# Kernel tuning notes

Hardware: AMD Instinct MI355X
Metric: run time of the kernel (lower is better)

Reference implementation:

```python
import jax, jax.numpy as jnp
import numpy as np

B, C, H_IMG, W_IMG = 16, 384, 56, 56
NUM_HEADS = 6
HEAD_DIM = C // NUM_HEADS
BN_EPS = 1e-5


def _bn(x, gamma, beta, mean, var):
    # x: [b, ch, n] or [b, ch, h, w]; per-channel affine normalization (eval-mode BatchNorm)
    shape = (1, -1) + (1,) * (x.ndim - 2)
    scale = (gamma / jnp.sqrt(var + BN_EPS)).reshape(shape)
    shift = (beta - mean * gamma / jnp.sqrt(var + BN_EPS)).reshape(shape)
    return x * scale + shift


def setup_inputs() -> dict:
    key = jax.random.key(0)
    ks = jax.random.split(key, 12)
    c2 = 2 * C
    return {
        "x": jax.random.normal(ks[0], (B, C, H_IMG, W_IMG), jnp.float32),
        "qk_w": jax.random.normal(ks[1], (c2, C // 2), jnp.float32) * 0.05,
        "qk_gamma": jax.random.uniform(ks[2], (c2,), jnp.float32, 0.5, 1.5),
        "qk_beta": jax.random.normal(ks[3], (c2,), jnp.float32) * 0.1,
        "qk_mean": jax.random.normal(ks[4], (c2,), jnp.float32) * 0.1,
        "qk_var": jax.random.uniform(ks[5], (c2,), jnp.float32, 0.5, 1.5),
        "pe_w": jax.random.normal(ks[6], (C, 1, 3, 3), jnp.float32) * 0.1,
        "pe_gamma": jax.random.uniform(ks[7], (C,), jnp.float32, 0.5, 1.5),
        "pe_beta": jax.random.normal(ks[8], (C,), jnp.float32) * 0.1,
        "pe_mean": jax.random.normal(ks[9], (C,), jnp.float32) * 0.1,
        "pe_var": jax.random.uniform(ks[10], (C,), jnp.float32, 0.5, 1.5),
    }


def reference(x, qk_w, qk_gamma, qk_beta, qk_mean, qk_var,
              pe_w, pe_gamma, pe_beta, pe_mean, pe_var):
    b, c, h, w = x.shape
    n = h * w
    s = n ** (-0.5)
    nh, hd = NUM_HEADS, HEAD_DIM

    # grouped (groups=2) 1x1 conv: out channels [0:c] from input [0:c/2], [c:2c] from [c/2:c]
    xg = x.reshape(b, 2, c // 2, n)                       # [b, 2, c/2, n]
    wg = qk_w.reshape(2, c, c // 2)                       # [group, out_per_group, in_per_group]
    qk = jnp.einsum('bgin,goi->bgon', xg, wg).reshape(b, 2 * c, n)
    qk = _bn(qk, qk_gamma, qk_beta, qk_mean, qk_var)
    qk = jax.nn.elu(qk) + 1.0

    qk = qk.reshape(b, 2, nh, hd, n)
    q, k = qk[:, 0], qk[:, 1]                             # [b, H, d, n]
    v = x.reshape(b, nh, hd, n)                           # [b, H, d, n]

    # kv = (k*s) @ (v^T * s): [b, H, d, d]
    kv = jnp.einsum('bhdn,bhen->bhde', k * s, v * s)
    # numerator: q^T @ kv -> [b, H, n, d]
    num = jnp.einsum('bhdn,bhde->bhne', q, kv)
    # denominator: q^T @ mean_n(k) -> [b, H, n]
    den = jnp.einsum('bhdn,bhd->bhn', q, k.mean(axis=-1)) + 1e-6
    attn = (num / den[..., None]).transpose(0, 1, 3, 2).reshape(b, c, h, w)

    # depthwise 3x3 conv positional encoding on v (= x) + BN
    pe = jax.lax.conv_general_dilated(
        x, pe_w, window_strides=(1, 1), padding=((1, 1), (1, 1)),
        feature_group_count=c, dimension_numbers=('NCHW', 'OIHW', 'NCHW'))
    pe = _bn(pe, pe_gamma, pe_beta, pe_mean, pe_var)

    return attn + pe
```

## Files before the change

kernel.cpp:

```cpp
#include <hip/hip_runtime.h>
#include <math.h>

#define N_SP 3136
#define BN_EPS 1e-5f

typedef __attribute__((ext_vector_type(8))) short short8;
typedef __attribute__((ext_vector_type(4))) float f32x4;

#define QK_SZ   (16*2*384*N_SP)
#define KVP_OFF (QK_SZ)
#define KVP_SZ  (16*6*7*64*64)
#define KMP_OFF (KVP_OFF + KVP_SZ)
#define KMP_SZ  (16*6*7*64)
#define KV_OFF  (KMP_OFF + KMP_SZ)
#define KV_SZ   (16*6*64*64)
#define KM_OFF  (KV_OFF + KV_SZ)
#define KM_SZ   (16*6*64)
#define WH_OFF  (KM_OFF + KM_SZ)
#define WSPLIT_N (2*384*192)

__device__ __forceinline__ void bsplit(float f, ushort& h, ushort& l) {
    uint u = __float_as_uint(f);
    uint hr = (u + 0x7FFFu + ((u >> 16) & 1u)) >> 16;
    h = (ushort)hr;
    float fh = __uint_as_float(hr << 16);
    float fl = f - fh;
    uint v = __float_as_uint(fl);
    l = (ushort)((v + 0x7FFFu + ((v >> 16) & 1u)) >> 16);
}

__global__ __launch_bounds__(256) void p0_wsplit(
    const float* __restrict__ qk_w, ushort* __restrict__ wh, ushort* __restrict__ wl)
{
    int idx = blockIdx.x * 256 + threadIdx.x;
    if (idx >= WSPLIT_N) return;
    ushort h, l;
    bsplit(qk_w[idx], h, l);
    wh[idx] = h;
    wl[idx] = l;
}

__global__ __launch_bounds__(256) void k1_qk_mfma(
    const float* __restrict__ x, const ushort* __restrict__ wh, const ushort* __restrict__ wl,
    const float* __restrict__ gamma, const float* __restrict__ beta,
    const float* __restrict__ mean, const float* __restrict__ var,
    float* __restrict__ qk_out)
{
    __shared__ __align__(16) ushort Ah[8192];
    __shared__ __align__(16) ushort Al[8192];
    __shared__ __align__(16) ushort Bh[4096];
    __shared__ __align__(16) ushort Bl[4096];

    const int bx = blockIdx.x;
    const int by = blockIdx.y;
    const int bz = blockIdx.z;
    const int b = bz >> 1, gg = bz & 1;
    const int t = threadIdx.x;
    const int lane = t & 63, wv = t >> 6;
    const int wr = wv >> 1, wc = wv & 1;
    const int lg = lane >> 4, l15 = lane & 15;

    f32x4 acc[4][2];
    #pragma unroll
    for (int m = 0; m < 4; ++m)
        #pragma unroll
        for (int nf = 0; nf < 2; ++nf)
            acc[m][nf] = (f32x4){0.f, 0.f, 0.f, 0.f};

    const float* xg = x + (size_t)(b * 384 + gg * 192) * N_SP + bx * 64;
    const ushort* whg = wh + (gg * 384 + by * 128) * 192;
    const ushort* wlg = wl + (gg * 384 + by * 128) * 192;

    for (int kt = 0; kt < 3; ++kt) {
        #pragma unroll
        for (int li = 0; li < 4; ++li) {
            int c = li * 256 + t;
            int row = c >> 3, kb = c & 7;
            int goff = row * 192 + kt * 64 + kb * 8;
            float4 vh = *(const float4*)(whg + goff);
            float4 vl = *(const float4*)(wlg + goff);
            int ch = (row * 8 + (kb ^ (row & 7))) * 8;
            *(float4*)&Ah[ch] = vh;
            *(float4*)&Al[ch] = vl;
        }
        #pragma unroll
        for (int li = 0; li < 2; ++li) {
            int idx = li * 256 + t;
            int kp = idx >> 4;
            int nq = idx & 15;
            int k0 = kp * 2;
            const float* px = xg + (size_t)(kt * 64 + k0) * N_SP + nq * 4;
            float4 v0 = *(const float4*)px;
            float4 v1 = *(const float4*)(px + N_SP);
            ushort h0[4], l0[4], h1[4], l1[4];
            float a0[4] = {v0.x, v0.y, v0.z, v0.w};
            float a1[4] = {v1.x, v1.y, v1.z, v1.w};
            #pragma unroll
            for (int i = 0; i < 4; ++i) { bsplit(a0[i], h0[i], l0[i]); bsplit(a1[i], h1[i], l1[i]); }
            int kb = k0 >> 3, ks = (k0 & 6) >> 1;
            #pragma unroll
            for (int i = 0; i < 4; ++i) {
                int n = nq * 4 + i;
                int chunk = n * 8 + (kb ^ ((n >> 1) & 7));
                ((uint*)Bh)[chunk * 4 + ks] = (uint)h0[i] | ((uint)h1[i] << 16);
                ((uint*)Bl)[chunk * 4 + ks] = (uint)l0[i] | ((uint)l1[i] << 16);
            }
        }
        __syncthreads();
        #pragma unroll
        for (int s = 0; s < 2; ++s) {
            short8 ah[4], al[4], bh[2], bl[2];
            int kb = s * 4 + lg;
            #pragma unroll
            for (int m = 0; m < 4; ++m) {
                int row = wr * 64 + m * 16 + l15;
                int ch = (row * 8 + (kb ^ (row & 7))) * 8;
                ah[m] = *(const short8*)&Ah[ch];
                al[m] = *(const short8*)&Al[ch];
            }
            #pragma unroll
            for (int nf = 0; nf < 2; ++nf) {
                int n = wc * 32 + nf * 16 + l15;
                int ch = (n * 8 + (kb ^ ((n >> 1) & 7))) * 8;
                bh[nf] = *(const short8*)&Bh[ch];
                bl[nf] = *(const short8*)&Bl[ch];
            }
            #pragma unroll
            for (int m = 0; m < 4; ++m)
                #pragma unroll
                for (int nf = 0; nf < 2; ++nf) {
                    acc[m][nf] = __builtin_amdgcn_mfma_f32_16x16x32_bf16(ah[m], bh[nf], acc[m][nf], 0, 0, 0);
                    acc[m][nf] = __builtin_amdgcn_mfma_f32_16x16x32_bf16(ah[m], bl[nf], acc[m][nf], 0, 0, 0);
                    acc[m][nf] = __builtin_amdgcn_mfma_f32_16x16x32_bf16(al[m], bh[nf], acc[m][nf], 0, 0, 0);
                }
        }
        __syncthreads();
    }

    float* scs = (float*)Bh;
    float* shs = scs + 128;
    if (t < 128) {
        int ch = gg * 384 + by * 128 + t;
        float sc = gamma[ch] / sqrtf(var[ch] + BN_EPS);
        scs[t] = sc;
        shs[t] = beta[ch] - mean[ch] * sc;
    }
    __syncthreads();

    size_t obase = ((size_t)(b * 2 + gg) * 384 + by * 128) * N_SP + bx * 64 + wc * 32;
    #pragma unroll
    for (int m = 0; m < 4; ++m)
        #pragma unroll
        for (int nf = 0; nf < 2; ++nf) {
            #pragma unroll
            for (int r = 0; r < 4; ++r) {
                int orow = wr * 64 + m * 16 + lg * 4 + r;
                float v = acc[m][nf][r] * scs[orow] + shs[orow];
                v = v > 0.f ? v + 1.f : __expf(v);
                qk_out[obase + (size_t)orow * N_SP + nf * 16 + l15] = v;
            }
        }
}

__global__ __launch_bounds__(256) void k2_kv(
    const float* __restrict__ x, const float* __restrict__ qk,
    float* __restrict__ kv_part, float* __restrict__ km_part)
{
    __shared__ float ks[64][68];
    __shared__ float vs[64][68];
    const int chunk = blockIdx.x;
    const int h = blockIdx.y, b = blockIdx.z;
    const int t = threadIdx.x, tx = t & 15, ty = t >> 4;
    const float* kp = qk + ((b*2+1)*384 + h*64)*N_SP;
    const float* vp = x  + (b*384 + h*64)*N_SP;
    float acc[4][4] = {};
    float kmacc[4] = {};
    for (int sub = 0; sub < 7; ++sub) {
        int n0 = chunk*448 + sub*64;
        #pragma unroll
        for (int l = 0; l < 4; ++l) {
            int idx = t + l*256;
            int d = idx >> 4, c = idx & 15;
            float4 v4 = *(const float4*)&kp[d*N_SP + n0 + c*4];
            ks[c*4+0][d] = v4.x; ks[c*4+1][d] = v4.y;
            ks[c*4+2][d] = v4.z; ks[c*4+3][d] = v4.w;
        }
        #pragma unroll
        for (int l = 0; l < 4; ++l) {
            int idx = t + l*256;
            int e = idx >> 4, c = idx & 15;
            float4 v4 = *(const float4*)&vp[e*N_SP + n0 + c*4];
            vs[c*4+0][e] = v4.x; vs[c*4+1][e] = v4.y;
            vs[c*4+2][e] = v4.z; vs[c*4+3][e] = v4.w;
        }
        __syncthreads();
        #pragma unroll 8
        for (int n = 0; n < 64; ++n) {
            float4 kd = *(const float4*)&ks[n][ty*4];
            float4 ve = *(const float4*)&vs[n][tx*4];
            float kk[4] = {kd.x,kd.y,kd.z,kd.w}, vv[4] = {ve.x,ve.y,ve.z,ve.w};
            #pragma unroll
            for (int i = 0; i < 4; ++i) {
                kmacc[i] += kk[i];
                #pragma unroll
                for (int j = 0; j < 4; ++j) acc[i][j] += kk[i]*vv[j];
            }
        }
        __syncthreads();
    }
    const int base = ((b*6+h)*7 + chunk)*4096;
    #pragma unroll
    for (int i = 0; i < 4; ++i) {
        float4 r = make_float4(acc[i][0], acc[i][1], acc[i][2], acc[i][3]);
        *(float4*)&kv_part[base + (ty*4+i)*64 + tx*4] = r;
    }
    if (tx == 0) {
        const int kb = ((b*6+h)*7 + chunk)*64;
        #pragma unroll
        for (int i = 0; i < 4; ++i) km_part[kb + ty*4+i] = kmacc[i];
    }
}

__global__ __launch_bounds__(256) void k2b_reduce(
    const float* __restrict__ kv_part, const float* __restrict__ km_part,
    float* __restrict__ kv, float* __restrict__ km)
{
    int idx = blockIdx.x*256 + threadIdx.x;
    const float inv_n = 1.0f / (float)N_SP;
    if (idx < 16*6*64*64) {
        int bh = idx >> 12, de = idx & 4095;
        float s = 0.f;
        #pragma unroll
        for (int c = 0; c < 7; ++c) s += kv_part[(bh*7+c)*4096 + de];
        kv[idx] = s * inv_n;
    }
    if (idx < 16*6*64) {
        int bh = idx >> 6, d = idx & 63;
        float s = 0.f;
        #pragma unroll
        for (int c = 0; c < 7; ++c) s += km_part[(bh*7+c)*64 + d];
        km[idx] = s * inv_n;
    }
}

__global__ __launch_bounds__(256) void k3_attn_pe(
    const float* __restrict__ x, const float* __restrict__ qk,
    const float* __restrict__ kv, const float* __restrict__ km,
    const float* __restrict__ pw,
    const float* __restrict__ pgamma, const float* __restrict__ pbeta,
    const float* __restrict__ pmean, const float* __restrict__ pvar,
    float* __restrict__ out)
{
    __shared__ float qs[64][68];
    __shared__ float kvs[64][68];
    __shared__ float kms[64];
    const int bx = blockIdx.x;
    const int h = blockIdx.y, b = blockIdx.z;
    const int t = threadIdx.x, tx = t & 15, ty = t >> 4;
    const int n0 = bx*64;
    const float* qp  = qk + ((b*2+0)*384 + h*64)*N_SP;
    const float* kvp = kv + (b*6+h)*4096;
    #pragma unroll
    for (int l = 0; l < 4; ++l) {
        int idx = t + l*256;
        int d = idx >> 4, c = idx & 15;
        *(float4*)&qs[d][c*4] = *(const float4*)&qp[d*N_SP + n0 + c*4];
    }
    #pragma unroll
    for (int l = 0; l < 4; ++l) {
        int idx = t + l*256;
        int d = idx >> 4, c = idx & 15;
        *(float4*)&kvs[d][c*4] = *(const float4*)&kvp[d*64 + c*4];
    }
    if (t < 64) kms[t] = km[(b*6+h)*64 + t];
    __syncthreads();

    float acc[4][4] = {};
    float den[4] = {};
    #pragma unroll 8
    for (int d = 0; d < 64; ++d) {
        float4 qn = *(const float4*)&qs[d][tx*4];
        float4 ke = *(const float4*)&kvs[d][ty*4];
        float qq[4] = {qn.x,qn.y,qn.z,qn.w}, kk[4] = {ke.x,ke.y,ke.z,ke.w};
        float kmd = kms[d];
        #pragma unroll
        for (int p = 0; p < 4; ++p) {
            den[p] += qq[p]*kmd;
            #pragma unroll
            for (int j = 0; j < 4; ++j) acc[p][j] += qq[p]*kk[j];
        }
    }

    const int p0 = n0 + tx*4;
    const int y = p0 / 56, xc = p0 % 56;
    #pragma unroll
    for (int j = 0; j < 4; ++j) {
        int c = h*64 + ty*4 + j;
        const float* xp = x + ((size_t)b*384 + c)*N_SP;
        float seg[3][6];
        #pragma unroll
        for (int dy = 0; dy < 3; ++dy) {
            int yy = y + dy - 1;
            bool yok = (yy >= 0) && (yy < 56);
            const float* xr = xp + yy*56;
            #pragma unroll
            for (int s = 0; s < 6; ++s) {
                int col = xc - 1 + s;
                seg[dy][s] = (yok && col >= 0 && col < 56) ? xr[col] : 0.f;
            }
        }
        float w9[9];
        #pragma unroll
        for (int q = 0; q < 9; ++q) w9[q] = pw[c*9 + q];
        float sc2 = pgamma[c] / sqrtf(pvar[c] + BN_EPS);
        float sh2 = pbeta[c] - pmean[c]*sc2;
        float4 r;
        float* pr = (float*)&r;
        #pragma unroll
        for (int p = 0; p < 4; ++p) {
            float conv = 0.f;
            #pragma unroll
            for (int dy = 0; dy < 3; ++dy)
                #pragma unroll
                for (int dx = 0; dx < 3; ++dx)
                    conv += w9[dy*3+dx] * seg[dy][p + dx];
            pr[p] = acc[p][j] / (den[p] + 1e-6f) + (conv*sc2 + sh2);
        }
        *(float4*)&out[((size_t)b*384 + c)*N_SP + p0] = r;
    }
}

extern "C" void kernel_launch(void* const* d_in, const int* in_sizes, int n_in,
                              void* d_out, int out_size, void* d_ws, size_t ws_size,
                              hipStream_t stream)
{
    const float* x        = (const float*)d_in[0];
    const float* qk_w     = (const float*)d_in[1];
    const float* qk_gamma = (const float*)d_in[2];
    const float* qk_beta  = (const float*)d_in[3];
    const float* qk_mean  = (const float*)d_in[4];
    const float* qk_var   = (const float*)d_in[5];
    const float* pe_w     = (const float*)d_in[6];
    const float* pe_gamma = (const float*)d_in[7];
    const float* pe_beta  = (const float*)d_in[8];
    const float* pe_mean  = (const float*)d_in[9];
    const float* pe_var   = (const float*)d_in[10];
    float* out = (float*)d_out;

    float* ws      = (float*)d_ws;
    float* qk      = ws;
    float* kv_part = ws + KVP_OFF;
    float* km_part = ws + KMP_OFF;
    float* kv      = ws + KV_OFF;
    float* km      = ws + KM_OFF;
    ushort* whp    = (ushort*)(ws + WH_OFF);
    ushort* wlp    = whp + WSPLIT_N;

    hipLaunchKernelGGL(p0_wsplit, dim3((WSPLIT_N + 255)/256), dim3(256), 0, stream,
                       qk_w, whp, wlp);
    dim3 g1(49, 3, 32);
    hipLaunchKernelGGL(k1_qk_mfma, g1, dim3(256), 0, stream,
                       x, whp, wlp, qk_gamma, qk_beta, qk_mean, qk_var, qk);
    dim3 g2(7, 6, 16);
    hipLaunchKernelGGL(k2_kv, g2, dim3(256), 0, stream, x, qk, kv_part, km_part);
    hipLaunchKernelGGL(k2b_reduce, dim3(1536), dim3(256), 0, stream,
                       kv_part, km_part, kv, km);
    dim3 g3(49, 6, 16);
    hipLaunchKernelGGL(k3_attn_pe, g3, dim3(256), 0, stream,
                       x, qk, kv, km, pe_w, pe_gamma, pe_beta, pe_mean, pe_var, out);
}
```

Baseline: 241.9 us.

## Compute KV with split-bf16 MFMA, fold k-mean into ones column, vectorize PE loads

```diff
diff --git a/kernel.cpp b/kernel.cpp
--- a/kernel.cpp
+++ b/kernel.cpp
@@ -9,10 +9,8 @@
 
 #define QK_SZ   (16*2*384*N_SP)
 #define KVP_OFF (QK_SZ)
-#define KVP_SZ  (16*6*7*64*64)
-#define KMP_OFF (KVP_OFF + KVP_SZ)
-#define KMP_SZ  (16*6*7*64)
-#define KV_OFF  (KMP_OFF + KMP_SZ)
+#define KVP_SZ  (16*6*7*64*80)
+#define KV_OFF  (KVP_OFF + KVP_SZ)
 #define KV_SZ   (16*6*64*64)
 #define KM_OFF  (KV_OFF + KV_SZ)
 #define KM_SZ   (16*6*64)
@@ -162,83 +160,106 @@
         }
 }
 
-__global__ __launch_bounds__(256) void k2_kv(
+__global__ __launch_bounds__(256) void k2_kv_mfma(
     const float* __restrict__ x, const float* __restrict__ qk,
-    float* __restrict__ kv_part, float* __restrict__ km_part)
-{
-    __shared__ float ks[64][68];
-    __shared__ float vs[64][68];
+    float* __restrict__ kv_part)
+{
+    __shared__ __align__(16) ushort Kh[4096], Kl[4096];
+    __shared__ __align__(16) ushort Vh[5120], Vl[5120];
+
     const int chunk = blockIdx.x;
     const int h = blockIdx.y, b = blockIdx.z;
-    const int t = threadIdx.x, tx = t & 15, ty = t >> 4;
-    const float* kp = qk + ((b*2+1)*384 + h*64)*N_SP;
-    const float* vp = x  + (b*384 + h*64)*N_SP;
-    float acc[4][4] = {};
-    float kmacc[4] = {};
+    const int t = threadIdx.x;
+    const int lane = t & 63, wv = t >> 6;
+    const int lg = lane >> 4, l15 = lane & 15;
+
+    const float* kp = qk + (size_t)((b*2+1)*384 + h*64) * N_SP;
+    const float* vp = x  + (size_t)(b*384 + h*64) * N_SP;
+
+    #pragma unroll
+    for (int li = 0; li < 4; ++li) {
+        int idx = li * 256 + t;
+        int row = 64 + (idx >> 6), col = idx & 63;
+        int off = (row * 8 + ((col >> 3) ^ (row & 7))) * 8 + (col & 7);
+        Vh[off] = (row == 64) ? (ushort)0x3F80 : (ushort)0;
+        Vl[off] = 0;
+    }
+
+    f32x4 acc[5];
+    #pragma unroll
+    for (int nf = 0; nf < 5; ++nf) acc[nf] = (f32x4){0.f, 0.f, 0.f, 0.f};
+
     for (int sub = 0; sub < 7; ++sub) {
-        int n0 = chunk*448 + sub*64;
-        #pragma unroll
-        for (int l = 0; l < 4; ++l) {
-            int idx = t + l*256;
-            int d = idx >> 4, c = idx & 15;
-            float4 v4 = *(const float4*)&kp[d*N_SP + n0 + c*4];
-            ks[c*4+0][d] = v4.x; ks[c*4+1][d] = v4.y;
-            ks[c*4+2][d] = v4.z; ks[c*4+3][d] = v4.w;
-        }
-        #pragma unroll
-        for (int l = 0; l < 4; ++l) {
-            int idx = t + l*256;
-            int e = idx >> 4, c = idx & 15;
-            float4 v4 = *(const float4*)&vp[e*N_SP + n0 + c*4];
-            vs[c*4+0][e] = v4.x; vs[c*4+1][e] = v4.y;
-            vs[c*4+2][e] = v4.z; vs[c*4+3][e] = v4.w;
+        int n0 = chunk * 448 + sub * 64;
+        #pragma unroll
+        for (int li = 0; li < 4; ++li) {
+            int idx = li * 256 + t;
+            int row = idx >> 4, sc = idx & 15;
+            int off = (row * 8 + ((sc >> 1) ^ (row & 7))) * 8 + (sc & 1) * 4;
+            float4 kf = *(const float4*)&kp[(size_t)row * N_SP + n0 + sc * 4];
+            ushort h0,h1,h2,h3,l0,l1,l2,l3;
+            bsplit(kf.x,h0,l0); bsplit(kf.y,h1,l1); bsplit(kf.z,h2,l2); bsplit(kf.w,h3,l3);
+            ((uint*)&Kh[off])[0] = (uint)h0 | ((uint)h1 << 16);
+            ((uint*)&Kh[off])[1] = (uint)h2 | ((uint)h3 << 16);
+            ((uint*)&Kl[off])[0] = (uint)l0 | ((uint)l1 << 16);
+            ((uint*)&Kl[off])[1] = (uint)l2 | ((uint)l3 << 16);
+            float4 vf = *(const float4*)&vp[(size_t)row * N_SP + n0 + sc * 4];
+            bsplit(vf.x,h0,l0); bsplit(vf.y,h1,l1); bsplit(vf.z,h2,l2); bsplit(vf.w,h3,l3);
+            ((uint*)&Vh[off])[0] = (uint)h0 | ((uint)h1 << 16);
+            ((uint*)&Vh[off])[1] = (uint)h2 | ((uint)h3 << 16);
+            ((uint*)&Vl[off])[0] = (uint)l0 | ((uint)l1 << 16);
+            ((uint*)&Vl[off])[1] = (uint)l2 | ((uint)l3 << 16);
         }
         __syncthreads();
-        #pragma unroll 8
-        for (int n = 0; n < 64; ++n) {
-            float4 kd = *(const float4*)&ks[n][ty*4];
-            float4 ve = *(const float4*)&vs[n][tx*4];
-            float kk[4] = {kd.x,kd.y,kd.z,kd.w}, vv[4] = {ve.x,ve.y,ve.z,ve.w};
-            #pragma unroll
-            for (int i = 0; i < 4; ++i) {
-                kmacc[i] += kk[i];
-                #pragma unroll
-                for (int j = 0; j < 4; ++j) acc[i][j] += kk[i]*vv[j];
+        #pragma unroll
+        for (int s = 0; s < 2; ++s) {
+            int arow = wv * 16 + l15;
+            int akb = (s * 4 + lg) ^ (arow & 7);
+            short8 ah = *(const short8*)&Kh[(arow * 8 + akb) * 8];
+            short8 al = *(const short8*)&Kl[(arow * 8 + akb) * 8];
+            #pragma unroll
+            for (int nf = 0; nf < 5; ++nf) {
+                int brow = nf * 16 + l15;
+                int bkb = (s * 4 + lg) ^ (brow & 7);
+                short8 bh = *(const short8*)&Vh[(brow * 8 + bkb) * 8];
+                short8 bl = *(const short8*)&Vl[(brow * 8 + bkb) * 8];
+                acc[nf] = __builtin_amdgcn_mfma_f32_16x16x32_bf16(ah, bh, acc[nf], 0, 0, 0);
+                acc[nf] = __builtin_amdgcn_mfma_f32_16x16x32_bf16(ah, bl, acc[nf], 0, 0, 0);
+                acc[nf] = __builtin_amdgcn_mfma_f32_16x16x32_bf16(al, bh, acc[nf], 0, 0, 0);
             }
         }
         __syncthreads();
     }
-    const int base = ((b*6+h)*7 + chunk)*4096;
-    #pragma unroll
-    for (int i = 0; i < 4; ++i) {
-        float4 r = make_float4(acc[i][0], acc[i][1], acc[i][2], acc[i][3]);
-        *(float4*)&kv_part[base + (ty*4+i)*64 + tx*4] = r;
-    }
-    if (tx == 0) {
-        const int kb = ((b*6+h)*7 + chunk)*64;
-        #pragma unroll
-        for (int i = 0; i < 4; ++i) km_part[kb + ty*4+i] = kmacc[i];
-    }
+
+    size_t base = (size_t)((b*6 + h)*7 + chunk) * 64 * 80;
+    #pragma unroll
+    for (int nf = 0; nf < 5; ++nf)
+        #pragma unroll
+        for (int r = 0; r < 4; ++r) {
+            int d = wv * 16 + lg * 4 + r;
+            kv_part[base + (size_t)d * 80 + nf * 16 + l15] = acc[nf][r];
+        }
 }
 
 __global__ __launch_bounds__(256) void k2b_reduce(
-    const float* __restrict__ kv_part, const float* __restrict__ km_part,
+    const float* __restrict__ kv_part,
     float* __restrict__ kv, float* __restrict__ km)
 {
     int idx = blockIdx.x*256 + threadIdx.x;
     const float inv_n = 1.0f / (float)N_SP;
     if (idx < 16*6*64*64) {
         int bh = idx >> 12, de = idx & 4095;
+        int d = de >> 6, e = de & 63;
         float s = 0.f;
         #pragma unroll
-        for (int c = 0; c < 7; ++c) s += kv_part[(bh*7+c)*4096 + de];
+        for (int c = 0; c < 7; ++c) s += kv_part[((size_t)(bh*7+c)*64 + d)*80 + e];
         kv[idx] = s * inv_n;
     }
     if (idx < 16*6*64) {
         int bh = idx >> 6, d = idx & 63;
         float s = 0.f;
         #pragma unroll
-        for (int c = 0; c < 7; ++c) s += km_part[(bh*7+c)*64 + d];
+        for (int c = 0; c < 7; ++c) s += kv_part[((size_t)(bh*7+c)*64 + d)*80 + 64];
         km[idx] = s * inv_n;
     }
 }
@@ -252,25 +273,18 @@
     float* __restrict__ out)
 {
     __shared__ float qs[64][68];
-    __shared__ float kvs[64][68];
     __shared__ float kms[64];
     const int bx = blockIdx.x;
     const int h = blockIdx.y, b = blockIdx.z;
     const int t = threadIdx.x, tx = t & 15, ty = t >> 4;
     const int n0 = bx*64;
-    const float* qp  = qk + ((b*2+0)*384 + h*64)*N_SP;
+    const float* qp  = qk + (size_t)((b*2+0)*384 + h*64)*N_SP;
     const float* kvp = kv + (b*6+h)*4096;
     #pragma unroll
     for (int l = 0; l < 4; ++l) {
         int idx = t + l*256;
         int d = idx >> 4, c = idx & 15;
-        *(float4*)&qs[d][c*4] = *(const float4*)&qp[d*N_SP + n0 + c*4];
-    }
-    #pragma unroll
-    for (int l = 0; l < 4; ++l) {
-        int idx = t + l*256;
-        int d = idx >> 4, c = idx & 15;
-        *(float4*)&kvs[d][c*4] = *(const float4*)&kvp[d*64 + c*4];
+        *(float4*)&qs[d][c*4] = *(const float4*)&qp[(size_t)d*N_SP + n0 + c*4];
     }
     if (t < 64) kms[t] = km[(b*6+h)*64 + t];
     __syncthreads();
@@ -280,7 +294,7 @@
     #pragma unroll 8
     for (int d = 0; d < 64; ++d) {
         float4 qn = *(const float4*)&qs[d][tx*4];
-        float4 ke = *(const float4*)&kvs[d][ty*4];
+        float4 ke = *(const float4*)&kvp[d*64 + ty*4];
         float qq[4] = {qn.x,qn.y,qn.z,qn.w}, kk[4] = {ke.x,ke.y,ke.z,ke.w};
         float kmd = kms[d];
         #pragma unroll
@@ -297,17 +311,21 @@
     for (int j = 0; j < 4; ++j) {
         int c = h*64 + ty*4 + j;
         const float* xp = x + ((size_t)b*384 + c)*N_SP;
-        float seg[3][6];
+        float s6[3][6];
         #pragma unroll
         for (int dy = 0; dy < 3; ++dy) {
             int yy = y + dy - 1;
             bool yok = (yy >= 0) && (yy < 56);
-            const float* xr = xp + yy*56;
-            #pragma unroll
-            for (int s = 0; s < 6; ++s) {
-                int col = xc - 1 + s;
-                seg[dy][s] = (yok && col >= 0 && col < 56) ? xr[col] : 0.f;
-            }
+            float4 mid = make_float4(0.f,0.f,0.f,0.f);
+            float lf = 0.f, rt = 0.f;
+            if (yok) {
+                const float* xr = xp + yy*56;
+                mid = *(const float4*)&xr[xc];
+                if (xc > 0)  lf = xr[xc-1];
+                if (xc < 52) rt = xr[xc+4];
+            }
+            s6[dy][0]=lf; s6[dy][1]=mid.x; s6[dy][2]=mid.y;
+            s6[dy][3]=mid.z; s6[dy][4]=mid.w; s6[dy][5]=rt;
         }
         float w9[9];
         #pragma unroll
@@ -323,7 +341,7 @@
             for (int dy = 0; dy < 3; ++dy)
                 #pragma unroll
                 for (int dx = 0; dx < 3; ++dx)
-                    conv += w9[dy*3+dx] * seg[dy][p + dx];
+                    conv += w9[dy*3+dx] * s6[dy][p + dx];
             pr[p] = acc[p][j] / (den[p] + 1e-6f) + (conv*sc2 + sh2);
         }
         *(float4*)&out[((size_t)b*384 + c)*N_SP + p0] = r;
@@ -350,7 +368,6 @@
     float* ws      = (float*)d_ws;
     float* qk      = ws;
     float* kv_part = ws + KVP_OFF;
-    float* km_part = ws + KMP_OFF;
     float* kv      = ws + KV_OFF;
     float* km      = ws + KM_OFF;
     ushort* whp    = (ushort*)(ws + WH_OFF);
@@ -362,9 +379,9 @@
     hipLaunchKernelGGL(k1_qk_mfma, g1, dim3(256), 0, stream,
                        x, whp, wlp, qk_gamma, qk_beta, qk_mean, qk_var, qk);
     dim3 g2(7, 6, 16);
-    hipLaunchKernelGGL(k2_kv, g2, dim3(256), 0, stream, x, qk, kv_part, km_part);
+    hipLaunchKernelGGL(k2_kv_mfma, g2, dim3(256), 0, stream, x, qk, kv_part);
     hipLaunchKernelGGL(k2b_reduce, dim3(1536), dim3(256), 0, stream,
-                       kv_part, km_part, kv, km);
+                       kv_part, kv, km);
     dim3 g3(49, 6, 16);
     hipLaunchKernelGGL(k3_attn_pe, g3, dim3(256), 0, stream,
                        x, qk, kv, km, pe_w, pe_gamma, pe_beta, pe_mean, pe_var, out);
```

New measurement: 219.8 us. -9.1%, faster.
